# Performance work log

Hardware: AMD Instinct MI355X
Metric: run time of the kernel (lower is better)

## Reference

```python
import jax, jax.numpy as jnp
import numpy as np

EMB_DIM = 512
NUM_HEADS = 8
HEAD_DIM = EMB_DIM // NUM_HEADS


def setup_inputs() -> dict:
    key = jax.random.key(0)
    ks = jax.random.split(key, 8)
    B, S, D = 2, 192, EMB_DIM
    return {
        "q": jax.random.normal(ks[0], (B, S, D), dtype=jnp.float32),
        "k": jax.random.normal(ks[1], (B, S, D), dtype=jnp.float32),
        "l": jax.random.normal(ks[2], (B, S, D), dtype=jnp.float32),
        "v": jax.random.normal(ks[3], (B, S, D), dtype=jnp.float32),
        "Wq": jax.random.normal(ks[4], (D, D), dtype=jnp.float32) * (1.0 / np.sqrt(D)),
        "Wk": jax.random.normal(ks[5], (D, D), dtype=jnp.float32) * (1.0 / np.sqrt(D)),
        "Wv": jax.random.normal(ks[6], (D, D), dtype=jnp.float32) * (1.0 / np.sqrt(D)),
        "Wout": jax.random.normal(ks[7], (D, D), dtype=jnp.float32) * (1.0 / np.sqrt(D)),
    }


def _heads(x, W):
    # torch nn.Linear: x @ W.T ; then split heads -> (B, H, S, hd)
    B, S, D = x.shape
    y = x @ W.T
    return y.reshape(B, S, NUM_HEADS, HEAD_DIM).transpose(0, 2, 1, 3)


def reference(q, k, l, v, Wq, Wk, Wv, Wout):
    B, QS, D = q.shape
    KS, LS = k.shape[1], l.shape[1]
    qh = _heads(q, Wq)
    kh = _heads(k, Wk)
    lh = _heads(l, Wk)  # NOTE: original module projects l with self.key (faithful)
    vh = _heads(v, Wv)
    # rank-3 attention scores: (B, H, QS, KS, LS)
    scores = jnp.einsum('bhqe,bhke,bhle->bhqkl', qh, kh, lh) / jnp.sqrt(
        jnp.asarray(HEAD_DIM, dtype=q.dtype))
    # softmax jointly over (KS, LS)
    attn = jax.nn.softmax(scores.reshape(B, NUM_HEADS, QS, KS * LS), axis=-1)
    attn = attn.reshape(B, NUM_HEADS, QS, KS, LS)
    # vv[b,h,l,k,d] = v[b,h,k,d]; contract over k and l -> (B, QS, H, hd)
    attended = jnp.einsum('bhqkl,bhkd->bqhd', attn, vh)
    concatenated = attended.reshape(B, QS, EMB_DIM)
    return concatenated @ Wout.T
```

## Files before the change

### kernel.cpp

```cpp
#include <hip/hip_runtime.h>
#include <math.h>

#define BB 2
#define SS 192
#define DD 512
#define HH 8
#define HD 64
#define QCB 6
#define NQC (SS / QCB)
#define PROJ_N (BB*HH*SS*HD)
#define SCL (0.125f * 1.44269504088896f)

typedef __attribute__((ext_vector_type(4))) float f32x4;
typedef _Float16 f16x8 __attribute__((ext_vector_type(8)));

__device__ __forceinline__ f16x8 cvt8_f16_rne(const float* g) {
    f16x8 r;
#pragma unroll
    for (int i = 0; i < 8; ++i) r[i] = (_Float16)g[i];
    return r;
}

__global__ __launch_bounds__(256) void zero_kernel(float* __restrict__ wsp,
                                                   float* __restrict__ out) {
    const int i = blockIdx.x * 256 + threadIdx.x;
    if (i < 4 * PROJ_N) wsp[i] = 0.f;
    if (i < BB * SS * DD) out[i] = 0.f;
}

__global__ __launch_bounds__(256) void proj4_kernel(
    const float* __restrict__ xq, const float* __restrict__ xk,
    const float* __restrict__ xl, const float* __restrict__ xv,
    const float* __restrict__ Wq, const float* __restrict__ Wk,
    const float* __restrict__ Wv, float* __restrict__ ws) {
    const int z = blockIdx.z;
    const int p = z >> 1;
    const int k0 = (z & 1) * 256;
    const float* x = (p == 0) ? xq : (p == 1) ? xk : (p == 2) ? xl : xv;
    const float* W = (p == 0) ? Wq : (p == 3) ? Wv : Wk;
    float* y = ws + p * PROJ_N;

    __shared__ short Ahs[2][4 * 64 * 8];
    __shared__ short Bhs[2][4 * 64 * 8];

    const int t = threadIdx.x;
    const int lane = t & 63, w = t >> 6;
    const int wr = w >> 1, wc = w & 1;
    const int c16 = lane & 15, q4 = lane >> 4;
    const int m0 = blockIdx.x * 64, n0 = blockIdx.y * 64;
    const int sr = t >> 2, scc = t & 3;

    f32x4 acc[2][2];
#pragma unroll
    for (int a = 0; a < 2; ++a)
#pragma unroll
        for (int b = 0; b < 2; ++b) acc[a][b] = (f32x4){0.f, 0.f, 0.f, 0.f};

#define STAGE(kk, bf)                                                              \
    {                                                                              \
        float a8[8], w8[8];                                                        \
        *(f32x4*)&a8[0] = *(const f32x4*)&x[(m0 + sr) * 512 + (kk) + scc * 8];     \
        *(f32x4*)&a8[4] = *(const f32x4*)&x[(m0 + sr) * 512 + (kk) + scc * 8 + 4]; \
        *(f32x4*)&w8[0] = *(const f32x4*)&W[(n0 + sr) * 512 + (kk) + scc * 8];     \
        *(f32x4*)&w8[4] = *(const f32x4*)&W[(n0 + sr) * 512 + (kk) + scc * 8 + 4]; \
        *(f16x8*)&Ahs[bf][(scc * 64 + sr) * 8] = cvt8_f16_rne(a8);                 \
        *(f16x8*)&Bhs[bf][(scc * 64 + sr) * 8] = cvt8_f16_rne(w8);                 \
    }

    STAGE(k0, 0)
    for (int s = 0; s < 8; ++s) {
        __syncthreads();
        if (s + 1 < 8) STAGE(k0 + (s + 1) * 32, (s + 1) & 1)
        const int b = s & 1;
        f16x8 aH[2], bH[2];
#pragma unroll
        for (int mt = 0; mt < 2; ++mt) {
            const int row = wr * 32 + mt * 16 + c16;
            aH[mt] = *(const f16x8*)&Ahs[b][(q4 * 64 + row) * 8];
        }
#pragma unroll
        for (int nt = 0; nt < 2; ++nt) {
            const int col = wc * 32 + nt * 16 + c16;
            bH[nt] = *(const f16x8*)&Bhs[b][(q4 * 64 + col) * 8];
        }
#pragma unroll
        for (int mt = 0; mt < 2; ++mt)
#pragma unroll
            for (int nt = 0; nt < 2; ++nt)
                acc[mt][nt] = __builtin_amdgcn_mfma_f32_16x16x32_f16(aH[mt], bH[nt], acc[mt][nt], 0, 0, 0);
    }
#undef STAGE

#pragma unroll
    for (int mt = 0; mt < 2; ++mt)
#pragma unroll
        for (int nt = 0; nt < 2; ++nt)
#pragma unroll
            for (int j = 0; j < 4; ++j) {
                const int n_row = m0 + wr * 32 + mt * 16 + q4 * 4 + j;
                const int col = n0 + wc * 32 + nt * 16 + c16;
                const int b = n_row / SS, s2 = n_row % SS;
                const int h = col >> 6, e = col & 63;
                atomicAdd(&y[((b * HH + h) * SS + s2) * HD + e], acc[mt][nt][j]);
            }
}

__global__ __launch_bounds__(512, 4) void attn3d_mfma_kernel(
    const float* __restrict__ qh, const float* __restrict__ kh,
    const float* __restrict__ lh, const float* __restrict__ vh,
    const float* __restrict__ Wout, float* __restrict__ out) {
    __shared__ short Kf16[8][193][8];
    __shared__ short Lf16[8][193][8];
    __shared__ short qpk[QCB][8][8];
    __shared__ float partial[2][QCB][196];
    __shared__ float Wt[QCB][192];
    __shared__ float attd[16][72];
    __shared__ float zinv[QCB];

    const int blk = blockIdx.x;
    const int bh = blk >> 5, qc = blk & 31;
    const int t = threadIdx.x;
    const int lane = t & 63, w = t >> 6;
    const int lg = w >> 2, kg = w & 3;
    const int c = lane & 15, eh = lane >> 4;

    if (t < QCB * 64) {
        const int q = t >> 6, e = t & 63;
        const float v = qh[(bh * SS + qc * QCB + q) * HD + e] * SCL;
        qpk[q][e >> 3][e & 7] = __builtin_bit_cast(short, (_Float16)v);
    }
#pragma unroll
    for (int j = 0; j < 3; ++j) {
        const int cid = t + 512 * j;
        const int k = cid >> 3, ec = cid & 7;
        float b8[8];
        const float* kp = &kh[(bh * SS + k) * HD + ec * 8];
        *(f32x4*)&b8[0] = *(const f32x4*)&kp[0];
        *(f32x4*)&b8[4] = *(const f32x4*)&kp[4];
        *(f16x8*)&Kf16[ec][k][0] = cvt8_f16_rne(b8);
        const float* lp = &lh[(bh * SS + k) * HD + ec * 8];
        *(f32x4*)&b8[0] = *(const f32x4*)&lp[0];
        *(f32x4*)&b8[4] = *(const f32x4*)&lp[4];
        *(f16x8*)&Lf16[ec][k][0] = cvt8_f16_rne(b8);
    }
    __syncthreads();

    for (int qpi = 0; qpi < 3; ++qpi) {
        const int qa = (qpi + w) % 3;
        const int qb = qa + 3;
        const f16x8 qaf0 = *(const f16x8*)&qpk[qa][eh][0];
        const f16x8 qaf1 = *(const f16x8*)&qpk[qa][4 + eh][0];
        const f16x8 qbf0 = *(const f16x8*)&qpk[qb][eh][0];
        const f16x8 qbf1 = *(const f16x8*)&qpk[qb][4 + eh][0];
        f16x8 Ba[3][2], Bb[3][2];
#pragma unroll
        for (int kt = 0; kt < 3; ++kt) {
            const int col = kg * 48 + kt * 16 + c;
            const f16x8 Kf0 = *(const f16x8*)&Kf16[eh][col][0];
            const f16x8 Kf1 = *(const f16x8*)&Kf16[4 + eh][col][0];
            Ba[kt][0] = Kf0 * qaf0;
            Ba[kt][1] = Kf1 * qaf1;
            Bb[kt][0] = Kf0 * qbf0;
            Bb[kt][1] = Kf1 * qbf1;
        }
        float ra0 = 0.f, ra1 = 0.f, ra2 = 0.f;
        float rb0 = 0.f, rb1 = 0.f, rb2 = 0.f;
#pragma unroll
        for (int lt = 0; lt < 6; ++lt) {
            const int row = lg * 96 + lt * 16 + c;
            const f16x8 A0 = *(const f16x8*)&Lf16[eh][row][0];
            const f16x8 A1 = *(const f16x8*)&Lf16[4 + eh][row][0];
            f32x4 a0 = (f32x4){0.f, 0.f, 0.f, 0.f};
            f32x4 a1 = (f32x4){0.f, 0.f, 0.f, 0.f};
            f32x4 a2 = (f32x4){0.f, 0.f, 0.f, 0.f};
            f32x4 b0 = (f32x4){0.f, 0.f, 0.f, 0.f};
            f32x4 b1 = (f32x4){0.f, 0.f, 0.f, 0.f};
            f32x4 b2 = (f32x4){0.f, 0.f, 0.f, 0.f};
            a0 = __builtin_amdgcn_mfma_f32_16x16x32_f16(A0, Ba[0][0], a0, 0, 0, 0);
            a1 = __builtin_amdgcn_mfma_f32_16x16x32_f16(A0, Ba[1][0], a1, 0, 0, 0);
            a2 = __builtin_amdgcn_mfma_f32_16x16x32_f16(A0, Ba[2][0], a2, 0, 0, 0);
            b0 = __builtin_amdgcn_mfma_f32_16x16x32_f16(A0, Bb[0][0], b0, 0, 0, 0);
            b1 = __builtin_amdgcn_mfma_f32_16x16x32_f16(A0, Bb[1][0], b1, 0, 0, 0);
            b2 = __builtin_amdgcn_mfma_f32_16x16x32_f16(A0, Bb[2][0], b2, 0, 0, 0);
            a0 = __builtin_amdgcn_mfma_f32_16x16x32_f16(A1, Ba[0][1], a0, 0, 0, 0);
            a1 = __builtin_amdgcn_mfma_f32_16x16x32_f16(A1, Ba[1][1], a1, 0, 0, 0);
            a2 = __builtin_amdgcn_mfma_f32_16x16x32_f16(A1, Ba[2][1], a2, 0, 0, 0);
            b0 = __builtin_amdgcn_mfma_f32_16x16x32_f16(A1, Bb[0][1], b0, 0, 0, 0);
            b1 = __builtin_amdgcn_mfma_f32_16x16x32_f16(A1, Bb[1][1], b1, 0, 0, 0);
            b2 = __builtin_amdgcn_mfma_f32_16x16x32_f16(A1, Bb[2][1], b2, 0, 0, 0);
            ra0 += (__builtin_amdgcn_exp2f(a0[0]) + __builtin_amdgcn_exp2f(a0[1])) +
                   (__builtin_amdgcn_exp2f(a0[2]) + __builtin_amdgcn_exp2f(a0[3]));
            ra1 += (__builtin_amdgcn_exp2f(a1[0]) + __builtin_amdgcn_exp2f(a1[1])) +
                   (__builtin_amdgcn_exp2f(a1[2]) + __builtin_amdgcn_exp2f(a1[3]));
            ra2 += (__builtin_amdgcn_exp2f(a2[0]) + __builtin_amdgcn_exp2f(a2[1])) +
                   (__builtin_amdgcn_exp2f(a2[2]) + __builtin_amdgcn_exp2f(a2[3]));
            rb0 += (__builtin_amdgcn_exp2f(b0[0]) + __builtin_amdgcn_exp2f(b0[1])) +
                   (__builtin_amdgcn_exp2f(b0[2]) + __builtin_amdgcn_exp2f(b0[3]));
            rb1 += (__builtin_amdgcn_exp2f(b1[0]) + __builtin_amdgcn_exp2f(b1[1])) +
                   (__builtin_amdgcn_exp2f(b1[2]) + __builtin_amdgcn_exp2f(b1[3]));
            rb2 += (__builtin_amdgcn_exp2f(b2[0]) + __builtin_amdgcn_exp2f(b2[1])) +
                   (__builtin_amdgcn_exp2f(b2[2]) + __builtin_amdgcn_exp2f(b2[3]));
        }
        ra0 += __shfl_xor(ra0, 16, 64);
        ra1 += __shfl_xor(ra1, 16, 64);
        ra2 += __shfl_xor(ra2, 16, 64);
        rb0 += __shfl_xor(rb0, 16, 64);
        rb1 += __shfl_xor(rb1, 16, 64);
        rb2 += __shfl_xor(rb2, 16, 64);
        ra0 += __shfl_xor(ra0, 32, 64);
        ra1 += __shfl_xor(ra1, 32, 64);
        ra2 += __shfl_xor(ra2, 32, 64);
        rb0 += __shfl_xor(rb0, 32, 64);
        rb1 += __shfl_xor(rb1, 32, 64);
        rb2 += __shfl_xor(rb2, 32, 64);
        if (eh == 0) {
            partial[lg][qa][kg * 48 + 0 * 16 + c] = ra0;
            partial[lg][qa][kg * 48 + 1 * 16 + c] = ra1;
            partial[lg][qa][kg * 48 + 2 * 16 + c] = ra2;
            partial[lg][qb][kg * 48 + 0 * 16 + c] = rb0;
            partial[lg][qb][kg * 48 + 1 * 16 + c] = rb1;
            partial[lg][qb][kg * 48 + 2 * 16 + c] = rb2;
        }
    }
    __syncthreads();

    for (int id = t; id < QCB * 192; id += 512) {
        const int q = id / 192, k = id - q * 192;
        Wt[q][k] = partial[0][q][k] + partial[1][q][k];
    }
    for (int id = t; id < 16 * 72; id += 512) ((float*)attd)[id] = 0.f;
    __syncthreads();

    if (w < QCB) {
        const int q = w;
        float z = Wt[q][lane] + Wt[q][lane + 64] + Wt[q][lane + 128];
#pragma unroll
        for (int off = 32; off >= 1; off >>= 1) z += __shfl_xor(z, off, 64);
        if (lane == 0) zinv[q] = 1.f / z;
    }
    __syncthreads();

    if (t < QCB * 64) {
        const int q = t >> 6, d = t & 63;
        const float* vp = vh + bh * SS * HD + d;
        float sum = 0.f;
        for (int k0 = 0; k0 < SS; k0 += 8) {
            float v8[8];
#pragma unroll
            for (int j = 0; j < 8; ++j) v8[j] = vp[(k0 + j) * HD];
#pragma unroll
            for (int j = 0; j < 8; ++j) sum = fmaf(Wt[q][k0 + j], v8[j], sum);
        }
        attd[q][d] = sum * zinv[q];
    }
    __syncthreads();

    const int b = bh >> 3, h = bh & 7;
    f16x8 Ae0, Ae1;
    {
        float a8[8];
        *(f32x4*)&a8[0] = *(const f32x4*)&attd[c][eh * 8];
        *(f32x4*)&a8[4] = *(const f32x4*)&attd[c][eh * 8 + 4];
        Ae0 = cvt8_f16_rne(a8);
        *(f32x4*)&a8[0] = *(const f32x4*)&attd[c][32 + eh * 8];
        *(f32x4*)&a8[4] = *(const f32x4*)&attd[c][32 + eh * 8 + 4];
        Ae1 = cvt8_f16_rne(a8);
    }
#pragma unroll
    for (int jt = 0; jt < 4; ++jt) {
        const int j = (w * 4 + jt) * 16 + c;
        const float* wp = &Wout[j * DD + h * HD];
        float b8[8];
        *(f32x4*)&b8[0] = *(const f32x4*)&wp[eh * 8];
        *(f32x4*)&b8[4] = *(const f32x4*)&wp[eh * 8 + 4];
        const f16x8 B0 = cvt8_f16_rne(b8);
        *(f32x4*)&b8[0] = *(const f32x4*)&wp[32 + eh * 8];
        *(f32x4*)&b8[4] = *(const f32x4*)&wp[32 + eh * 8 + 4];
        const f16x8 B1 = cvt8_f16_rne(b8);
        f32x4 oc = (f32x4){0.f, 0.f, 0.f, 0.f};
        oc = __builtin_amdgcn_mfma_f32_16x16x32_f16(Ae0, B0, oc, 0, 0, 0);
        oc = __builtin_amdgcn_mfma_f32_16x16x32_f16(Ae1, B1, oc, 0, 0, 0);
#pragma unroll
        for (int jj = 0; jj < 4; ++jj) {
            const int q = eh * 4 + jj;
            if (q < QCB)
                atomicAdd(&out[(b * SS + qc * QCB + q) * DD + (w * 4 + jt) * 16 + c], oc[jj]);
        }
    }
}

extern "C" void kernel_launch(void* const* d_in, const int* in_sizes, int n_in,
                              void* d_out, int out_size, void* d_ws, size_t ws_size,
                              hipStream_t stream) {
    (void)in_sizes; (void)n_in; (void)out_size; (void)ws_size;
    const float* q    = (const float*)d_in[0];
    const float* k    = (const float*)d_in[1];
    const float* l    = (const float*)d_in[2];
    const float* v    = (const float*)d_in[3];
    const float* Wq   = (const float*)d_in[4];
    const float* Wk   = (const float*)d_in[5];
    const float* Wv   = (const float*)d_in[6];
    const float* Wout = (const float*)d_in[7];
    float* out = (float*)d_out;

    float* ws  = (float*)d_ws;
    float* qhp = ws + 0 * PROJ_N;
    float* khp = ws + 1 * PROJ_N;
    float* lhp = ws + 2 * PROJ_N;
    float* vhp = ws + 3 * PROJ_N;

    zero_kernel<<<dim3((4 * PROJ_N + 255) / 256), 256, 0, stream>>>(ws, out);
    proj4_kernel<<<dim3(384 / 64, 512 / 64, 8), 256, 0, stream>>>(
        q, k, l, v, Wq, Wk, Wv, ws);
    attn3d_mfma_kernel<<<dim3(16 * NQC), 512, 0, stream>>>(qhp, khp, lhp, vhp, Wout, out);
}
```

Before: 48.42 us.

## Drop split-K atomics in projection and fold output zeroing into it

The projection GEMM no longer splits K across two blocks, so each block covers the full K=512 with a 64-wide K step and two MFMAs per tile, and writes results with plain stores instead of atomicAdd. Because the workspace no longer needs zeroing, the separate zero kernel is removed and the output buffer (still accumulated atomically by the attention kernel) is zeroed inside the projection kernel with a grid-stride loop. This saves one kernel launch, the workspace memset and the atomic traffic. In exchange the grid has half as many blocks (192), so there is less parallelism per launch.

```diff
diff --git a/kernel.cpp b/kernel.cpp
--- a/kernel.cpp
+++ b/kernel.cpp
@@ -21,34 +21,32 @@
     return r;
 }
 
-__global__ __launch_bounds__(256) void zero_kernel(float* __restrict__ wsp,
-                                                   float* __restrict__ out) {
-    const int i = blockIdx.x * 256 + threadIdx.x;
-    if (i < 4 * PROJ_N) wsp[i] = 0.f;
-    if (i < BB * SS * DD) out[i] = 0.f;
-}
-
 __global__ __launch_bounds__(256) void proj4_kernel(
     const float* __restrict__ xq, const float* __restrict__ xk,
     const float* __restrict__ xl, const float* __restrict__ xv,
     const float* __restrict__ Wq, const float* __restrict__ Wk,
-    const float* __restrict__ Wv, float* __restrict__ ws) {
-    const int z = blockIdx.z;
-    const int p = z >> 1;
-    const int k0 = (z & 1) * 256;
+    const float* __restrict__ Wv, float* __restrict__ ws,
+    float* __restrict__ out) {
+    const int p = blockIdx.z;
     const float* x = (p == 0) ? xq : (p == 1) ? xk : (p == 2) ? xl : xv;
     const float* W = (p == 0) ? Wq : (p == 3) ? Wv : Wk;
     float* y = ws + p * PROJ_N;
 
-    __shared__ short Ahs[2][4 * 64 * 8];
-    __shared__ short Bhs[2][4 * 64 * 8];
+    __shared__ short Ahs[2][8 * 64 * 8];
+    __shared__ short Bhs[2][8 * 64 * 8];
 
     const int t = threadIdx.x;
+
+    {
+        const int bid = (blockIdx.z * gridDim.y + blockIdx.y) * gridDim.x + blockIdx.x;
+        for (int i = bid * 256 + t; i < BB * SS * DD; i += 192 * 256) out[i] = 0.f;
+    }
+
     const int lane = t & 63, w = t >> 6;
     const int wr = w >> 1, wc = w & 1;
     const int c16 = lane & 15, q4 = lane >> 4;
     const int m0 = blockIdx.x * 64, n0 = blockIdx.y * 64;
-    const int sr = t >> 2, scc = t & 3;
+    const int r = t >> 2, cc = t & 3;
 
     f32x4 acc[2][2];
 #pragma unroll
@@ -56,38 +54,45 @@
 #pragma unroll
         for (int b = 0; b < 2; ++b) acc[a][b] = (f32x4){0.f, 0.f, 0.f, 0.f};
 
-#define STAGE(kk, bf)                                                              \
-    {                                                                              \
-        float a8[8], w8[8];                                                        \
-        *(f32x4*)&a8[0] = *(const f32x4*)&x[(m0 + sr) * 512 + (kk) + scc * 8];     \
-        *(f32x4*)&a8[4] = *(const f32x4*)&x[(m0 + sr) * 512 + (kk) + scc * 8 + 4]; \
-        *(f32x4*)&w8[0] = *(const f32x4*)&W[(n0 + sr) * 512 + (kk) + scc * 8];     \
-        *(f32x4*)&w8[4] = *(const f32x4*)&W[(n0 + sr) * 512 + (kk) + scc * 8 + 4]; \
-        *(f16x8*)&Ahs[bf][(scc * 64 + sr) * 8] = cvt8_f16_rne(a8);                 \
-        *(f16x8*)&Bhs[bf][(scc * 64 + sr) * 8] = cvt8_f16_rne(w8);                 \
-    }
-
-    STAGE(k0, 0)
+#define STAGE(kk, bf)                                                               \
+    {                                                                               \
+        _Pragma("unroll") for (int h2 = 0; h2 < 2; ++h2) {                          \
+            const int ec = cc * 2 + h2;                                             \
+            float a8[8], w8[8];                                                     \
+            *(f32x4*)&a8[0] = *(const f32x4*)&x[(m0 + r) * 512 + (kk) + ec * 8];    \
+            *(f32x4*)&a8[4] = *(const f32x4*)&x[(m0 + r) * 512 + (kk) + ec * 8 + 4];\
+            *(f32x4*)&w8[0] = *(const f32x4*)&W[(n0 + r) * 512 + (kk) + ec * 8];    \
+            *(f32x4*)&w8[4] = *(const f32x4*)&W[(n0 + r) * 512 + (kk) + ec * 8 + 4];\
+            *(f16x8*)&Ahs[bf][(ec * 64 + r) * 8] = cvt8_f16_rne(a8);                \
+            *(f16x8*)&Bhs[bf][(ec * 64 + r) * 8] = cvt8_f16_rne(w8);                \
+        }                                                                           \
+    }
+
+    STAGE(0, 0)
     for (int s = 0; s < 8; ++s) {
         __syncthreads();
-        if (s + 1 < 8) STAGE(k0 + (s + 1) * 32, (s + 1) & 1)
+        if (s + 1 < 8) STAGE((s + 1) * 64, (s + 1) & 1)
         const int b = s & 1;
-        f16x8 aH[2], bH[2];
+        f16x8 aH[2][2], bH[2][2];
 #pragma unroll
         for (int mt = 0; mt < 2; ++mt) {
             const int row = wr * 32 + mt * 16 + c16;
-            aH[mt] = *(const f16x8*)&Ahs[b][(q4 * 64 + row) * 8];
+            aH[mt][0] = *(const f16x8*)&Ahs[b][(q4 * 64 + row) * 8];
+            aH[mt][1] = *(const f16x8*)&Ahs[b][((q4 + 4) * 64 + row) * 8];
         }
 #pragma unroll
         for (int nt = 0; nt < 2; ++nt) {
             const int col = wc * 32 + nt * 16 + c16;
-            bH[nt] = *(const f16x8*)&Bhs[b][(q4 * 64 + col) * 8];
+            bH[nt][0] = *(const f16x8*)&Bhs[b][(q4 * 64 + col) * 8];
+            bH[nt][1] = *(const f16x8*)&Bhs[b][((q4 + 4) * 64 + col) * 8];
         }
 #pragma unroll
         for (int mt = 0; mt < 2; ++mt)
 #pragma unroll
-            for (int nt = 0; nt < 2; ++nt)
-                acc[mt][nt] = __builtin_amdgcn_mfma_f32_16x16x32_f16(aH[mt], bH[nt], acc[mt][nt], 0, 0, 0);
+            for (int nt = 0; nt < 2; ++nt) {
+                acc[mt][nt] = __builtin_amdgcn_mfma_f32_16x16x32_f16(aH[mt][0], bH[nt][0], acc[mt][nt], 0, 0, 0);
+                acc[mt][nt] = __builtin_amdgcn_mfma_f32_16x16x32_f16(aH[mt][1], bH[nt][1], acc[mt][nt], 0, 0, 0);
+            }
     }
 #undef STAGE
 
@@ -101,7 +106,7 @@
                 const int col = n0 + wc * 32 + nt * 16 + c16;
                 const int b = n_row / SS, s2 = n_row % SS;
                 const int h = col >> 6, e = col & 63;
-                atomicAdd(&y[((b * HH + h) * SS + s2) * HD + e], acc[mt][nt][j]);
+                y[((b * HH + h) * SS + s2) * HD + e] = acc[mt][nt][j];
             }
 }
 
@@ -309,8 +314,7 @@
     float* lhp = ws + 2 * PROJ_N;
     float* vhp = ws + 3 * PROJ_N;
 
-    zero_kernel<<<dim3((4 * PROJ_N + 255) / 256), 256, 0, stream>>>(ws, out);
-    proj4_kernel<<<dim3(384 / 64, 512 / 64, 8), 256, 0, stream>>>(
-        q, k, l, v, Wq, Wk, Wv, ws);
+    proj4_kernel<<<dim3(384 / 64, 512 / 64, 4), 256, 0, stream>>>(
+        q, k, l, v, Wq, Wk, Wv, ws, out);
     attn3d_mfma_kernel<<<dim3(16 * NQC), 512, 0, stream>>>(qhp, khp, lhp, vhp, Wout, out);
 }
```

Measured after the change: 43.28 us. 10.6% less time.
